# Performance work log

Hardware: AMD Instinct MI355X
Metric: run time of the kernel (lower is better)

The kernel has to match this reference:

```python
import jax, jax.numpy as jnp
import numpy as np

K_BINS = 8192
HIDDEN = 2048
SQRT2 = 1.4142135623730951
LEAKY_SLOPE = 0.01
TMIN = 1e-10


def setup_inputs() -> dict:
    key = jax.random.key(0)
    k0, k1, k2 = jax.random.split(key, 3)
    D = 2 * K_BINS  # mu length so that cat([mu, t]) has 2K+1 features
    # positive mu keeps mu ** (gamma - 1/(1-gamma)) (a fractional power) finite
    mu = jax.random.uniform(k0, (D,), jnp.float32, 0.1, 1.0)
    t = jnp.array([0.5], jnp.float32)
    gamma = jnp.array([0.5], jnp.float32)  # 1/(1-gamma) = 2 -> integral exponent
    W1 = jax.random.normal(k1, (D + 1, HIDDEN), jnp.float32) * (1.0 / np.sqrt(D + 1))
    b1 = jnp.zeros((HIDDEN,), jnp.float32)
    W2 = jax.random.normal(k2, (HIDDEN, D), jnp.float32) * (1.0 / np.sqrt(HIDDEN))
    b2 = jnp.zeros((D,), jnp.float32)
    return {"mu": mu, "t": t, "gamma": gamma, "W1": W1, "b1": b1,
            "W2": W2, "b2": b2, "K": K_BINS}


def reference(mu, t, gamma, W1, b1, W2, b2, K):
    g = gamma[0]
    # --- NN(cat([mu, t])) -> (mu_epsilon, ln_sigma_epsilon), each [K] ---
    inp = jnp.concatenate([mu, t])                      # [2K+1]
    h = jax.nn.leaky_relu(inp @ W1 + b1, LEAKY_SLOPE)   # [hidden]
    out = h @ W2 + b2                                   # [2K]
    mu_eps, ln_sig = out[:K], out[K:]
    # --- mu_x / sigma_x (t < tmin branch folded in via where) ---
    p_mu = g - 1.0 / (1.0 - g)
    p_eps = 1.0 / (1.0 - g)
    mu_x_nn = jnp.power(mu[:K], p_mu) * jnp.power(mu_eps, p_eps)
    sigma_x_nn = jnp.power(1.0 - g, -0.5) * jnp.exp(0.5 * ln_sig)
    use_nn = t[0] >= TMIN
    mu_x = jnp.where(use_nn, mu_x_nn, jnp.zeros_like(mu_eps))     # [K]
    sigma_x = jnp.where(use_nn, sigma_x_nn, jnp.ones_like(mu_eps))  # [K]
    # --- vectorized discretised CDF differences over the (D_out, K) grid ---
    kk = jnp.arange(K, dtype=jnp.float32)
    kl = 2.0 * (kk - 1.0) / (K - 1.0)   # left bin edges  [K]
    kr = 2.0 * kk / (K - 1.0)           # right bin edges [K]

    def cdf(x):  # x: [K] edges -> G: [D_out, K]
        z = (x[None, :] - mu_x[:, None]) / (sigma_x[:, None] * SQRT2)
        F = 0.5 * (1.0 + jax.lax.erf(z))
        return jnp.where(x[None, :] <= -1.0, 0.0,
                         jnp.where(x[None, :] >= 1.0, 1.0, F))

    return cdf(kr) - cdf(kl)  # [K, K] per-bin probabilities
```

## Files before the change

kernel.cpp:

```cpp
#include <hip/hip_runtime.h>
#include <math.h>

#define KBINS 8192
#define DDIM  16384
#define HID   2048
#define LASTROW 16384

#define C1 16
#define NB1 1024
#define C2 16
#define NB2 128

static constexpr float SQRT2_F  = 1.4142135623730951f;
static constexpr float INVSQ2PI = 0.3989422804014327f;

__device__ __forceinline__ float fast_erff(float x) {
    float ax = fabsf(x);
    float t  = 1.0f / fmaf(0.3275911f, ax, 1.0f);
    float p  = t * (0.254829592f +
               t * (-0.284496736f +
               t * (1.421413741f +
               t * (-1.453152027f +
               t * 1.061405429f))));
    float r = 1.0f - p * __expf(-ax * ax);
    return copysignf(r, x);
}

__global__ void __launch_bounds__(256, 8)
mv1_partial(const float* __restrict__ mu, const float* __restrict__ W1,
            float* __restrict__ part1) {
    __shared__ float a_s[C1];
    int r0 = blockIdx.y * C1;
    if (threadIdx.x < C1) a_s[threadIdx.x] = mu[r0 + threadIdx.x];
    __syncthreads();
    int c0 = (blockIdx.x * 256 + threadIdx.x) * 4;
    float4 acc0 = {0.f, 0.f, 0.f, 0.f};
    float4 acc1 = {0.f, 0.f, 0.f, 0.f};
    const float* wp = W1 + (size_t)r0 * HID + c0;
#pragma unroll
    for (int k = 0; k < C1; k += 2) {
        float a0 = a_s[k];
        float a1 = a_s[k + 1];
        const float4 w0 = *reinterpret_cast<const float4*>(wp + (size_t)k * HID);
        const float4 w1 = *reinterpret_cast<const float4*>(wp + (size_t)(k + 1) * HID);
        acc0.x += a0 * w0.x; acc0.y += a0 * w0.y; acc0.z += a0 * w0.z; acc0.w += a0 * w0.w;
        acc1.x += a1 * w1.x; acc1.y += a1 * w1.y; acc1.z += a1 * w1.z; acc1.w += a1 * w1.w;
    }
    float4 acc = {acc0.x + acc1.x, acc0.y + acc1.y, acc0.z + acc1.z, acc0.w + acc1.w};
    *reinterpret_cast<float4*>(part1 + (size_t)blockIdx.y * HID + c0) = acc;
}

__global__ void __launch_bounds__(256)
h_reduce(const float* __restrict__ part1, const float* __restrict__ b1,
         const float* __restrict__ W1, const float* __restrict__ t,
         float* __restrict__ h) {
    __shared__ float red[4][64];
    int lane = threadIdx.x & 63;
    int sub  = threadIdx.x >> 6;
    int col  = blockIdx.x * 64 + lane;
    float s = 0.f;
#pragma unroll 8
    for (int rb = sub; rb < NB1; rb += 4)
        s += part1[(size_t)rb * HID + col];
    red[sub][lane] = s;
    __syncthreads();
    if (threadIdx.x < 64) {
        int c = blockIdx.x * 64 + threadIdx.x;
        float v = b1[c] + t[0] * W1[(size_t)LASTROW * HID + c];
        v += red[0][threadIdx.x] + red[1][threadIdx.x]
           + red[2][threadIdx.x] + red[3][threadIdx.x];
        h[c] = (v >= 0.f) ? v : 0.01f * v;
    }
}

__global__ void __launch_bounds__(256, 8)
mv2_partial(const float* __restrict__ h, const float* __restrict__ W2,
            float* __restrict__ part2) {
    __shared__ float hs[C2];
    int r0 = blockIdx.y * C2;
    if (threadIdx.x < C2) hs[threadIdx.x] = h[r0 + threadIdx.x];
    __syncthreads();
    int c0 = (blockIdx.x * 256 + threadIdx.x) * 4;
    float4 acc0 = {0.f, 0.f, 0.f, 0.f};
    float4 acc1 = {0.f, 0.f, 0.f, 0.f};
    const float* wp = W2 + (size_t)r0 * DDIM + c0;
#pragma unroll
    for (int k = 0; k < C2; k += 2) {
        float a0 = hs[k];
        float a1 = hs[k + 1];
        const float4 w0 = *reinterpret_cast<const float4*>(wp + (size_t)k * DDIM);
        const float4 w1 = *reinterpret_cast<const float4*>(wp + (size_t)(k + 1) * DDIM);
        acc0.x += a0 * w0.x; acc0.y += a0 * w0.y; acc0.z += a0 * w0.z; acc0.w += a0 * w0.w;
        acc1.x += a1 * w1.x; acc1.y += a1 * w1.y; acc1.z += a1 * w1.z; acc1.w += a1 * w1.w;
    }
    float4 acc = {acc0.x + acc1.x, acc0.y + acc1.y, acc0.z + acc1.z, acc0.w + acc1.w};
    *reinterpret_cast<float4*>(part2 + (size_t)blockIdx.y * DDIM + c0) = acc;
}

__global__ void __launch_bounds__(256)
scalars(const float* __restrict__ part2, const float* __restrict__ b2,
        const float* __restrict__ mu, const float* __restrict__ t,
        const float* __restrict__ gamma,
        float* __restrict__ mu_x, float* __restrict__ sigma_x) {
    int i = blockIdx.x * 256 + threadIdx.x;
    float s0 = b2[i];
    float s1 = b2[i + KBINS];
#pragma unroll 8
    for (int rb = 0; rb < NB2; ++rb) {
        s0 += part2[(size_t)rb * DDIM + i];
        s1 += part2[(size_t)rb * DDIM + i + KBINS];
    }
    float g  = gamma[0];
    float pe = 1.0f / (1.0f - g);
    float pm = g - pe;
    bool use_nn = (t[0] >= 1e-10f);
    float mx = powf(mu[i], pm) * powf(s0, pe);
    float sx = powf(1.0f - g, -0.5f) * expf(0.5f * s1);
    mu_x[i]    = use_nn ? mx : 0.0f;
    sigma_x[i] = use_nn ? sx : 1.0f;
}

__global__ void __launch_bounds__(256, 8)
cdf_row(const float* __restrict__ mu_x, const float* __restrict__ sigma_x,
        float* __restrict__ out) {
    int tid = threadIdx.x;
#pragma unroll
    for (int rr = 0; rr < 4; ++rr) {
        int i = blockIdx.x + rr * 2048;
        float m    = mu_x[i];
        float invs = 1.0f / sigma_x[i];
        const float sc = 2.0f / 8191.0f;
        float A    = sc * invs;
        float B    = (-1.0f / 8191.0f - m) * invs;
        float coef = INVSQ2PI * A;
        float* orow = out + (size_t)i * KBINS;
#pragma unroll
        for (int it = 0; it < 8; ++it) {
            int j0 = it * 1024 + tid * 4;
            float4 r;
            if (j0 < 4096) {
                float u0 = fmaf((float)j0, A, B);
                float u1 = u0 + A;
                float u2 = u1 + A;
                float u3 = u2 + A;
                r.x = coef * __expf(-0.5f * u0 * u0);
                r.y = coef * __expf(-0.5f * u1 * u1);
                r.z = coef * __expf(-0.5f * u2 * u2);
                r.w = coef * __expf(-0.5f * u3 * u3);
            } else if (j0 == 4096) {
                float z = (8190.0f / 8191.0f - m) * invs * (1.0f / SQRT2_F);
                r.x = 0.5f * (1.0f - fast_erff(z));
                r.y = r.z = r.w = 0.f;
            } else {
                r.x = r.y = r.z = r.w = 0.f;
            }
            *reinterpret_cast<float4*>(orow + j0) = r;
        }
    }
}

extern "C" void kernel_launch(void* const* d_in, const int* in_sizes, int n_in,
                              void* d_out, int out_size, void* d_ws, size_t ws_size,
                              hipStream_t stream) {
    const float* mu    = (const float*)d_in[0];
    const float* t     = (const float*)d_in[1];
    const float* gamma = (const float*)d_in[2];
    const float* W1    = (const float*)d_in[3];
    const float* b1    = (const float*)d_in[4];
    const float* W2    = (const float*)d_in[5];
    const float* b2    = (const float*)d_in[6];
    float* out = (float*)d_out;

    float* ws      = (float*)d_ws;
    float* part1   = ws;
    float* h       = part1 + (size_t)NB1 * HID;
    float* part2   = h + HID;
    float* mu_x    = part2 + (size_t)NB2 * DDIM;
    float* sigma_x = mu_x + KBINS;

    mv1_partial<<<dim3(2, NB1),  dim3(256), 0, stream>>>(mu, W1, part1);
    h_reduce   <<<dim3(32),      dim3(256), 0, stream>>>(part1, b1, W1, t, h);
    mv2_partial<<<dim3(16, NB2), dim3(256), 0, stream>>>(h, W2, part2);
    scalars    <<<dim3(32),      dim3(256), 0, stream>>>(part2, b2, mu, t, gamma, mu_x, sigma_x);
    cdf_row    <<<dim3(2048),    dim3(256), 0, stream>>>(mu_x, sigma_x, out);
}
```

Measured before the change: 165.5 us.

## Fuse hidden reduction into second matvec and widen reduction parallelism

Removes the separate h_reduce kernel: each mv2 block recomputes its own 8 hidden activations by reducing the part1 partials, then runs its slice of the W2 matvec. mv1 now has each block cover all columns for a 16-row chunk, and mv2 splits into 256 row chunks with 8 column groups per thread. The scalars reduction gets 256 blocks that split the partial sums across threads and combine them in shared memory, and cdf_row is relaunched with 4096 blocks of 2 rows each. The exchange is one fewer launch and more parallel reductions, at the cost of recomputing part of the hidden reduction in every mv2 block and a larger part2 buffer.

After: 144.2 us. -12.9%, faster.

```diff
diff --git a/kernel.cpp b/kernel.cpp
--- a/kernel.cpp
+++ b/kernel.cpp
@@ -8,8 +8,8 @@
 
 #define C1 16
 #define NB1 1024
-#define C2 16
-#define NB2 128
+#define C2 8
+#define NB2 256
 
 static constexpr float SQRT2_F  = 1.4142135623730951f;
 static constexpr float INVSQ2PI = 0.3989422804014327f;
@@ -26,75 +26,77 @@
     return copysignf(r, x);
 }
 
-__global__ void __launch_bounds__(256, 8)
+__global__ void __launch_bounds__(256)
 mv1_partial(const float* __restrict__ mu, const float* __restrict__ W1,
             float* __restrict__ part1) {
     __shared__ float a_s[C1];
-    int r0 = blockIdx.y * C1;
+    int r0 = blockIdx.x * C1;
     if (threadIdx.x < C1) a_s[threadIdx.x] = mu[r0 + threadIdx.x];
     __syncthreads();
-    int c0 = (blockIdx.x * 256 + threadIdx.x) * 4;
+    int c0 = threadIdx.x * 4;
     float4 acc0 = {0.f, 0.f, 0.f, 0.f};
     float4 acc1 = {0.f, 0.f, 0.f, 0.f};
-    const float* wp = W1 + (size_t)r0 * HID + c0;
-#pragma unroll
-    for (int k = 0; k < C1; k += 2) {
-        float a0 = a_s[k];
-        float a1 = a_s[k + 1];
-        const float4 w0 = *reinterpret_cast<const float4*>(wp + (size_t)k * HID);
-        const float4 w1 = *reinterpret_cast<const float4*>(wp + (size_t)(k + 1) * HID);
-        acc0.x += a0 * w0.x; acc0.y += a0 * w0.y; acc0.z += a0 * w0.z; acc0.w += a0 * w0.w;
-        acc1.x += a1 * w1.x; acc1.y += a1 * w1.y; acc1.z += a1 * w1.z; acc1.w += a1 * w1.w;
-    }
-    float4 acc = {acc0.x + acc1.x, acc0.y + acc1.y, acc0.z + acc1.z, acc0.w + acc1.w};
-    *reinterpret_cast<float4*>(part1 + (size_t)blockIdx.y * HID + c0) = acc;
-}
-
-__global__ void __launch_bounds__(256)
-h_reduce(const float* __restrict__ part1, const float* __restrict__ b1,
-         const float* __restrict__ W1, const float* __restrict__ t,
-         float* __restrict__ h) {
-    __shared__ float red[4][64];
-    int lane = threadIdx.x & 63;
-    int sub  = threadIdx.x >> 6;
-    int col  = blockIdx.x * 64 + lane;
-    float s = 0.f;
+    const float* wp = W1 + (size_t)r0 * HID;
+#pragma unroll
+    for (int k = 0; k < C1; ++k) {
+        float a = a_s[k];
+        const float4 w0 = *reinterpret_cast<const float4*>(wp + (size_t)k * HID + c0);
+        const float4 w1 = *reinterpret_cast<const float4*>(wp + (size_t)k * HID + c0 + 1024);
+        acc0.x += a * w0.x; acc0.y += a * w0.y; acc0.z += a * w0.z; acc0.w += a * w0.w;
+        acc1.x += a * w1.x; acc1.y += a * w1.y; acc1.z += a * w1.z; acc1.w += a * w1.w;
+    }
+    float* pp = part1 + (size_t)blockIdx.x * HID;
+    *reinterpret_cast<float4*>(pp + c0)        = acc0;
+    *reinterpret_cast<float4*>(pp + c0 + 1024) = acc1;
+}
+
+__global__ void __launch_bounds__(256)
+mv2h(const float* __restrict__ part1, const float* __restrict__ b1,
+     const float* __restrict__ W1, const float* __restrict__ t,
+     const float* __restrict__ W2, float* __restrict__ part2) {
+    __shared__ float red[32][8];
+    __shared__ float hs[C2];
+    int r0    = blockIdx.y * C2;
+    int cbase = blockIdx.x * 8192;
+    int col_l = threadIdx.x & 7;
+    int sub   = threadIdx.x >> 3;
+    {
+        float s = 0.f;
+        const float* p = part1 + r0 + col_l;
 #pragma unroll 8
-    for (int rb = sub; rb < NB1; rb += 4)
-        s += part1[(size_t)rb * HID + col];
-    red[sub][lane] = s;
-    __syncthreads();
-    if (threadIdx.x < 64) {
-        int c = blockIdx.x * 64 + threadIdx.x;
-        float v = b1[c] + t[0] * W1[(size_t)LASTROW * HID + c];
-        v += red[0][threadIdx.x] + red[1][threadIdx.x]
-           + red[2][threadIdx.x] + red[3][threadIdx.x];
-        h[c] = (v >= 0.f) ? v : 0.01f * v;
-    }
-}
-
-__global__ void __launch_bounds__(256, 8)
-mv2_partial(const float* __restrict__ h, const float* __restrict__ W2,
-            float* __restrict__ part2) {
-    __shared__ float hs[C2];
-    int r0 = blockIdx.y * C2;
-    if (threadIdx.x < C2) hs[threadIdx.x] = h[r0 + threadIdx.x];
-    __syncthreads();
-    int c0 = (blockIdx.x * 256 + threadIdx.x) * 4;
-    float4 acc0 = {0.f, 0.f, 0.f, 0.f};
-    float4 acc1 = {0.f, 0.f, 0.f, 0.f};
-    const float* wp = W2 + (size_t)r0 * DDIM + c0;
-#pragma unroll
-    for (int k = 0; k < C2; k += 2) {
-        float a0 = hs[k];
-        float a1 = hs[k + 1];
-        const float4 w0 = *reinterpret_cast<const float4*>(wp + (size_t)k * DDIM);
-        const float4 w1 = *reinterpret_cast<const float4*>(wp + (size_t)(k + 1) * DDIM);
-        acc0.x += a0 * w0.x; acc0.y += a0 * w0.y; acc0.z += a0 * w0.z; acc0.w += a0 * w0.w;
-        acc1.x += a1 * w1.x; acc1.y += a1 * w1.y; acc1.z += a1 * w1.z; acc1.w += a1 * w1.w;
-    }
-    float4 acc = {acc0.x + acc1.x, acc0.y + acc1.y, acc0.z + acc1.z, acc0.w + acc1.w};
-    *reinterpret_cast<float4*>(part2 + (size_t)blockIdx.y * DDIM + c0) = acc;
+        for (int m = 0; m < 32; ++m)
+            s += p[(size_t)(sub + (m << 5)) * HID];
+        red[sub][col_l] = s;
+    }
+    __syncthreads();
+    if (threadIdx.x < C2) {
+        int r = r0 + threadIdx.x;
+        float v = b1[r] + t[0] * W1[(size_t)LASTROW * HID + r];
+#pragma unroll
+        for (int p = 0; p < 32; ++p) v += red[p][threadIdx.x];
+        hs[threadIdx.x] = (v >= 0.f) ? v : 0.01f * v;
+    }
+    __syncthreads();
+    int c0 = threadIdx.x * 4;
+    float4 acc[8];
+#pragma unroll
+    for (int q = 0; q < 8; ++q) acc[q] = {0.f, 0.f, 0.f, 0.f};
+    const float* wp = W2 + (size_t)r0 * DDIM + cbase + c0;
+#pragma unroll 2
+    for (int k = 0; k < C2; ++k) {
+        float a = hs[k];
+        const float* wr = wp + (size_t)k * DDIM;
+#pragma unroll
+        for (int q = 0; q < 8; ++q) {
+            const float4 w = *reinterpret_cast<const float4*>(wr + q * 1024);
+            acc[q].x += a * w.x; acc[q].y += a * w.y;
+            acc[q].z += a * w.z; acc[q].w += a * w.w;
+        }
+    }
+    float* pp = part2 + (size_t)blockIdx.y * DDIM + cbase + c0;
+#pragma unroll
+    for (int q = 0; q < 8; ++q)
+        *reinterpret_cast<float4*>(pp + q * 1024) = acc[q];
 }
 
 __global__ void __launch_bounds__(256)
@@ -102,31 +104,46 @@
         const float* __restrict__ mu, const float* __restrict__ t,
         const float* __restrict__ gamma,
         float* __restrict__ mu_x, float* __restrict__ sigma_x) {
-    int i = blockIdx.x * 256 + threadIdx.x;
-    float s0 = b2[i];
-    float s1 = b2[i + KBINS];
+    __shared__ float red0[8][32];
+    __shared__ float red1[8][32];
+    int col_l = threadIdx.x & 31;
+    int sub   = threadIdx.x >> 5;
+    int c     = blockIdx.x * 32 + col_l;
+    float s0 = 0.f, s1 = 0.f;
+    const float* p0 = part2 + c;
+    const float* p1 = part2 + c + KBINS;
 #pragma unroll 8
-    for (int rb = 0; rb < NB2; ++rb) {
-        s0 += part2[(size_t)rb * DDIM + i];
-        s1 += part2[(size_t)rb * DDIM + i + KBINS];
-    }
-    float g  = gamma[0];
-    float pe = 1.0f / (1.0f - g);
-    float pm = g - pe;
-    bool use_nn = (t[0] >= 1e-10f);
-    float mx = powf(mu[i], pm) * powf(s0, pe);
-    float sx = powf(1.0f - g, -0.5f) * expf(0.5f * s1);
-    mu_x[i]    = use_nn ? mx : 0.0f;
-    sigma_x[i] = use_nn ? sx : 1.0f;
-}
-
-__global__ void __launch_bounds__(256, 8)
+    for (int m = 0; m < 32; ++m) {
+        size_t off = (size_t)(sub + (m << 3)) * DDIM;
+        s0 += p0[off];
+        s1 += p1[off];
+    }
+    red0[sub][col_l] = s0;
+    red1[sub][col_l] = s1;
+    __syncthreads();
+    if (threadIdx.x < 32) {
+        int cc = blockIdx.x * 32 + threadIdx.x;
+        float v0 = b2[cc];
+        float v1 = b2[cc + KBINS];
+#pragma unroll
+        for (int p = 0; p < 8; ++p) { v0 += red0[p][threadIdx.x]; v1 += red1[p][threadIdx.x]; }
+        float g  = gamma[0];
+        float pe = 1.0f / (1.0f - g);
+        float pm = g - pe;
+        bool use_nn = (t[0] >= 1e-10f);
+        float mx = powf(mu[cc], pm) * powf(v0, pe);
+        float sx = powf(1.0f - g, -0.5f) * expf(0.5f * v1);
+        mu_x[cc]    = use_nn ? mx : 0.0f;
+        sigma_x[cc] = use_nn ? sx : 1.0f;
+    }
+}
+
+__global__ void __launch_bounds__(256)
 cdf_row(const float* __restrict__ mu_x, const float* __restrict__ sigma_x,
         float* __restrict__ out) {
     int tid = threadIdx.x;
-#pragma unroll
-    for (int rr = 0; rr < 4; ++rr) {
-        int i = blockIdx.x + rr * 2048;
+    for (int rr = 0; rr < 2; ++rr) {
+        int i = blockIdx.x * 2 + rr;
         float m    = mu_x[i];
         float invs = 1.0f / sigma_x[i];
         const float sc = 2.0f / 8191.0f;
@@ -173,14 +190,12 @@
 
     float* ws      = (float*)d_ws;
     float* part1   = ws;
-    float* h       = part1 + (size_t)NB1 * HID;
-    float* part2   = h + HID;
+    float* part2   = part1 + (size_t)NB1 * HID;
     float* mu_x    = part2 + (size_t)NB2 * DDIM;
     float* sigma_x = mu_x + KBINS;
 
-    mv1_partial<<<dim3(2, NB1),  dim3(256), 0, stream>>>(mu, W1, part1);
-    h_reduce   <<<dim3(32),      dim3(256), 0, stream>>>(part1, b1, W1, t, h);
-    mv2_partial<<<dim3(16, NB2), dim3(256), 0, stream>>>(h, W2, part2);
-    scalars    <<<dim3(32),      dim3(256), 0, stream>>>(part2, b2, mu, t, gamma, mu_x, sigma_x);
-    cdf_row    <<<dim3(2048),    dim3(256), 0, stream>>>(mu_x, sigma_x, out);
-}
+    mv1_partial<<<dim3(NB1),     dim3(256), 0, stream>>>(mu, W1, part1);
+    mv2h       <<<dim3(2, NB2),  dim3(256), 0, stream>>>(part1, b1, W1, t, W2, part2);
+    scalars    <<<dim3(256),     dim3(256), 0, stream>>>(part2, b2, mu, t, gamma, mu_x, sigma_x);
+    cdf_row    <<<dim3(4096),    dim3(256), 0, stream>>>(mu_x, sigma_x, out);
+}
```
